# Kernel optimization log

Hardware: AMD Instinct MI355X
Metric: run time of the kernel (lower is better)

The kernel has to match this reference:

```python
import jax, jax.numpy as jnp
import numpy as np

# --- MLA config (DeepSeek-V3 style, scaled) ---
HIDDEN = 4096
N_HEADS = 32
Q_LORA = 1536
KV_LORA = 512
ROPE_D = 64
NOPE_D = 128
V_D = 128
Q_HEAD_D = NOPE_D + ROPE_D  # 192
EPS = 1e-6
SCALING = Q_HEAD_D ** (-0.5)
ROPE_THETA = 10000.0
B, S = 1, 2048


def rms_norm(x, w):
    var = jnp.mean(jnp.square(x.astype(jnp.float32)), axis=-1, keepdims=True)
    return (x * jax.lax.rsqrt(var + EPS)).astype(x.dtype) * w


def rotate_half(x):
    x1, x2 = jnp.split(x, 2, axis=-1)
    return jnp.concatenate([-x2, x1], axis=-1)


def apply_rope(x, cos, sin):
    # x: [B, H, S, ROPE_D]; cos/sin: [B, S, ROPE_D] -> unsqueeze head dim
    c = cos[:, None, :, :]
    s = sin[:, None, :, :]
    return x * c + rotate_half(x) * s


def setup_inputs() -> dict:
    key = jax.random.key(0)
    ks = jax.random.split(key, 8)
    hidden_states = jax.random.normal(ks[0], (B, S, HIDDEN), dtype=jnp.float32)
    # real RoPE tables
    inv_freq = 1.0 / (ROPE_THETA ** (np.arange(0, ROPE_D, 2, dtype=np.float32) / ROPE_D))
    t = np.arange(S, dtype=np.float32)
    freqs = np.outer(t, inv_freq)                      # [S, ROPE_D/2]
    emb = np.concatenate([freqs, freqs], axis=-1)      # [S, ROPE_D]
    cos = jnp.asarray(np.cos(emb))[None].repeat(B, 0)  # [B, S, ROPE_D]
    sin = jnp.asarray(np.sin(emb))[None].repeat(B, 0)
    scale = lambda fan_in: 1.0 / np.sqrt(fan_in)
    w_q_a = jax.random.normal(ks[1], (Q_LORA, HIDDEN), dtype=jnp.float32) * scale(HIDDEN)
    q_a_ln_w = jnp.ones((Q_LORA,), dtype=jnp.float32)
    w_q_b = jax.random.normal(ks[2], (N_HEADS * Q_HEAD_D, Q_LORA), dtype=jnp.float32) * scale(Q_LORA)
    w_kv_a = jax.random.normal(ks[3], (KV_LORA + ROPE_D, HIDDEN), dtype=jnp.float32) * scale(HIDDEN)
    kv_a_ln_w = jnp.ones((KV_LORA,), dtype=jnp.float32)
    w_kv_b = jax.random.normal(ks[4], (N_HEADS * (NOPE_D + V_D), KV_LORA), dtype=jnp.float32) * scale(KV_LORA)
    w_o = jax.random.normal(ks[5], (HIDDEN, N_HEADS * V_D), dtype=jnp.float32) * scale(N_HEADS * V_D)
    return {
        'hidden_states': hidden_states, 'cos': cos, 'sin': sin,
        'w_q_a': w_q_a, 'q_a_ln_w': q_a_ln_w, 'w_q_b': w_q_b,
        'w_kv_a': w_kv_a, 'kv_a_ln_w': kv_a_ln_w, 'w_kv_b': w_kv_b, 'w_o': w_o,
    }


def reference(hidden_states, cos, sin, w_q_a, q_a_ln_w, w_q_b, w_kv_a, kv_a_ln_w, w_kv_b, w_o):
    b, s, _ = hidden_states.shape
    # --- Q path: low-rank down + RMSNorm + up ---
    q_lat = rms_norm(hidden_states @ w_q_a.T, q_a_ln_w)              # [B,S,Q_LORA]
    q = (q_lat @ w_q_b.T).reshape(b, s, N_HEADS, Q_HEAD_D)
    q = q.transpose(0, 2, 1, 3)                                       # [B,H,S,Q_HEAD_D]
    q_nope, q_rot = q[..., :NOPE_D], q[..., NOPE_D:]                  # (note: source names swapped)
    # --- KV path: shared compressed latent + single rotary key ---
    ckv = hidden_states @ w_kv_a.T                                    # [B,S,KV_LORA+ROPE_D]
    k_lat, k_rot = ckv[..., :KV_LORA], ckv[..., KV_LORA:]
    kv = (rms_norm(k_lat, kv_a_ln_w) @ w_kv_b.T).reshape(b, s, N_HEADS, NOPE_D + V_D)
    kv = kv.transpose(0, 2, 1, 3)                                     # [B,H,S,NOPE_D+V_D]
    k_nope, v = kv[..., :NOPE_D], kv[..., NOPE_D:]
    k_rot = k_rot.reshape(b, 1, s, ROPE_D)                            # single rotary key head
    # --- partial RoPE on rotary slices ---
    q_rot = apply_rope(q_rot, cos, sin)
    k_rot = apply_rope(k_rot, cos, sin)
    k_rot = jnp.broadcast_to(k_rot, (b, N_HEADS, s, ROPE_D))
    query = jnp.concatenate([q_rot, q_nope], axis=-1)                 # [B,H,S,192]
    key = jnp.concatenate([k_rot, k_nope], axis=-1)                   # [B,H,S,192]
    # --- eager causal attention ---
    scores = jnp.einsum('bhqd,bhkd->bhqk', query, key) * SCALING
    causal = jnp.tril(jnp.ones((s, s), dtype=bool))
    scores = jnp.where(causal[None, None], scores, jnp.finfo(scores.dtype).min)
    probs = jax.nn.softmax(scores, axis=-1)
    attn = jnp.einsum('bhqk,bhkd->bhqd', probs, v)                    # [B,H,S,V_D]
    attn = attn.transpose(0, 2, 1, 3).reshape(b, s, N_HEADS * V_D)
    return attn @ w_o.T                                               # [B,S,HIDDEN]
```

## Files before the change

### kernel.cpp

```cpp
#include <hip/hip_runtime.h>

typedef unsigned short u16;
typedef u16 u16x4 __attribute__((ext_vector_type(4)));
typedef u16 u16x8 __attribute__((ext_vector_type(8)));
typedef float f32x4 __attribute__((ext_vector_type(4)));
typedef __bf16 bf16x8 __attribute__((ext_vector_type(8)));

#define S_LEN 2048
#define HIDDEN_D 4096
#define NHEADS 32
#define QLORA 1536
#define KVLORA 512
#define ROPED 64
#define NOPED 128
#define VDIM 128
#define QHD 192
#define SCALING_F 0.07216878364870323f

__device__ __forceinline__ u16 f2bf(float x) {
  union { float f; unsigned u; } v; v.f = x;
  unsigned r = v.u + 0x7fffu + ((v.u >> 16) & 1u);
  return (u16)(r >> 16);
}

__device__ __forceinline__ f32x4 mfma_bf16(u16x8 a, u16x8 b, f32x4 c) {
  return __builtin_amdgcn_mfma_f32_16x16x32_bf16(
      __builtin_bit_cast(bf16x8, a), __builtin_bit_cast(bf16x8, b), c, 0, 0, 0);
}

__global__ __launch_bounds__(256) void cvt_kernel(const float* __restrict__ in,
                                                  u16* __restrict__ out, int n4) {
  int i = blockIdx.x * 256 + threadIdx.x;
  if (i >= n4) return;
  f32x4 v = ((const f32x4*)in)[i];
  u16x4 o;
  o[0] = f2bf(v[0]); o[1] = f2bf(v[1]); o[2] = f2bf(v[2]); o[3] = f2bf(v[3]);
  ((u16x4*)out)[i] = o;
}

__global__ __launch_bounds__(256, 2) void gemm_kernel(
    const u16* __restrict__ A, const float* __restrict__ B, float* __restrict__ C,
    int M, int N, int K, int lda, int ldb, int ldc)
{
  __shared__ u16 sA[2][128 * 64];
  __shared__ u16 sB[2][128 * 64];
  const int tid = threadIdx.x;
  const int wid = tid >> 6, lane = tid & 63;
  const int lr = lane & 15, lg = lane >> 4;
  const int nbn = (N + 127) >> 7;
  const int bx = blockIdx.x % nbn, by = blockIdx.x / nbn;
  const int bm = by << 7, bn = bx << 7;
  const int wm = (wid >> 1) << 6, wn = (wid & 1) << 6;

  f32x4 acc[4][4] = {};
  u16x8 areg[4];
  f32x4 br0[4], br1[4];

  auto loadA = [&](int k0) {
#pragma unroll
    for (int i = 0; i < 4; ++i) {
      int chunk = i * 256 + tid;
      int row = chunk >> 3, c8 = chunk & 7;
      int gr = bm + row; if (gr >= M) gr = M - 1;
      areg[i] = *(const u16x8*)(A + (size_t)gr * lda + k0 + (c8 << 3));
    }
  };
  auto loadB = [&](int k0) {
#pragma unroll
    for (int i = 0; i < 4; ++i) {
      int chunk = i * 256 + tid;
      int n = chunk >> 3, c8 = chunk & 7;
      int gn = bn + n; if (gn >= N) gn = N - 1;
      const float* src = B + (size_t)gn * ldb + k0 + (c8 << 3);
      br0[i] = *(const f32x4*)src;
      br1[i] = *(const f32x4*)(src + 4);
    }
  };
  auto writeA = [&](int buf) {
#pragma unroll
    for (int i = 0; i < 4; ++i)
      *(u16x8*)&sA[buf][(i * 256 + tid) * 8] = areg[i];
  };
  auto writeB = [&](int buf) {
#pragma unroll
    for (int i = 0; i < 4; ++i) {
      u16x8 v;
      v[0] = f2bf(br0[i][0]); v[1] = f2bf(br0[i][1]);
      v[2] = f2bf(br0[i][2]); v[3] = f2bf(br0[i][3]);
      v[4] = f2bf(br1[i][0]); v[5] = f2bf(br1[i][1]);
      v[6] = f2bf(br1[i][2]); v[7] = f2bf(br1[i][3]);
      *(u16x8*)&sB[buf][(i * 256 + tid) * 8] = v;
    }
  };
  auto compute = [&](int buf) {
    const u16* pa = sA[buf];
    const u16* pb = sB[buf];
#pragma unroll
    for (int ks = 0; ks < 2; ++ks) {
      const int kof = ks * 32 + lg * 8;
      u16x8 av[4], bv[4];
#pragma unroll
      for (int m = 0; m < 4; ++m) av[m] = *(const u16x8*)&pa[(wm + m * 16 + lr) * 64 + kof];
#pragma unroll
      for (int n = 0; n < 4; ++n) bv[n] = *(const u16x8*)&pb[(wn + n * 16 + lr) * 64 + kof];
#pragma unroll
      for (int m = 0; m < 4; ++m)
#pragma unroll
        for (int n = 0; n < 4; ++n)
          acc[m][n] = mfma_bf16(av[m], bv[n], acc[m][n]);
    }
  };

  const int nk = K >> 6;
  loadA(0); loadB(0);
  writeA(0); writeB(0);
  __syncthreads();
  for (int t = 0; t < nk; ++t) {
    const int cur = t & 1;
    if (t + 1 < nk) { loadA((t + 1) << 6); loadB((t + 1) << 6); }
    compute(cur);
    if (t + 1 < nk) { writeA(cur ^ 1); writeB(cur ^ 1); }
    __syncthreads();
  }
#pragma unroll
  for (int m = 0; m < 4; ++m) {
    const int row0 = bm + wm + m * 16 + (lg << 2);
#pragma unroll
    for (int n = 0; n < 4; ++n) {
      const int col = bn + wn + n * 16 + lr;
      if (col < N) {
#pragma unroll
        for (int r = 0; r < 4; ++r)
          C[(size_t)(row0 + r) * ldc + col] = acc[m][n][r];
      }
    }
  }
}

__global__ __launch_bounds__(256) void rms_kernel(const float* __restrict__ X,
                                                  const float* __restrict__ w,
                                                  u16* __restrict__ out, int D) {
  const int row = blockIdx.x;
  const float* x = X + (size_t)row * D;
  __shared__ float sb[4];
  float ss = 0.f;
  for (int i = threadIdx.x * 4; i < D; i += 1024) {
    f32x4 v = *(const f32x4*)&x[i];
    ss += v[0] * v[0] + v[1] * v[1] + v[2] * v[2] + v[3] * v[3];
  }
#pragma unroll
  for (int off = 32; off >= 1; off >>= 1) ss += __shfl_xor(ss, off, 64);
  if ((threadIdx.x & 63) == 0) sb[threadIdx.x >> 6] = ss;
  __syncthreads();
  const float inv = rsqrtf((sb[0] + sb[1] + sb[2] + sb[3]) / (float)D + 1e-6f);
  u16* o = out + (size_t)row * D;
  for (int i = threadIdx.x * 4; i < D; i += 1024) {
    f32x4 v = *(const f32x4*)&x[i];
    f32x4 wv = *(const f32x4*)&w[i];
    u16x4 u;
    u[0] = f2bf(v[0] * inv * wv[0]); u[1] = f2bf(v[1] * inv * wv[1]);
    u[2] = f2bf(v[2] * inv * wv[2]); u[3] = f2bf(v[3] * inv * wv[3]);
    *(u16x4*)&o[i] = u;
  }
}

__global__ __launch_bounds__(256) void ckv_epi_kernel(const float* __restrict__ ckv,
    const float* __restrict__ w, const float* __restrict__ cosp, const float* __restrict__ sinp,
    u16* __restrict__ klatn, u16* __restrict__ krot) {
  const int s = blockIdx.x;
  const float* x = ckv + (size_t)s * 576;
  __shared__ float sb[4];
  const int i2 = threadIdx.x * 2;
  const float a = x[i2], b = x[i2 + 1];
  float ss = a * a + b * b;
#pragma unroll
  for (int off = 32; off >= 1; off >>= 1) ss += __shfl_xor(ss, off, 64);
  if ((threadIdx.x & 63) == 0) sb[threadIdx.x >> 6] = ss;
  __syncthreads();
  const float inv = rsqrtf((sb[0] + sb[1] + sb[2] + sb[3]) / 512.0f + 1e-6f);
  klatn[(size_t)s * 512 + i2]     = f2bf(a * inv * w[i2]);
  klatn[(size_t)s * 512 + i2 + 1] = f2bf(b * inv * w[i2 + 1]);
  if (threadIdx.x < 64) {
    const int d = threadIdx.x;
    const float xr = x[512 + d];
    const float rr = (d < 32) ? -x[512 + d + 32] : x[512 + d - 32];
    krot[(size_t)s * 64 + d] = f2bf(xr * cosp[s * 64 + d] + rr * sinp[s * 64 + d]);
  }
}

__global__ __launch_bounds__(256) void q_epi_kernel(const float* __restrict__ q_raw,
    const float* __restrict__ cosp, const float* __restrict__ sinp, u16* __restrict__ Qb) {
  const int s = blockIdx.x;
  const float* x = q_raw + (size_t)s * 6144;
  for (int idx = threadIdx.x; idx < 6144; idx += 256) {
    const int h = idx / 192, d = idx - h * 192;
    float v;
    if (d < 64) {
      const float xr = x[h * 192 + 128 + d];
      const float rr = (d < 32) ? -x[h * 192 + 160 + d] : x[h * 192 + 96 + d];
      v = xr * cosp[s * 64 + d] + rr * sinp[s * 64 + d];
    } else {
      v = x[h * 192 + d - 64];
    }
    Qb[((size_t)h * 2048 + s) * QHD + d] = f2bf(v * SCALING_F);
  }
}

__global__ __launch_bounds__(256) void kv_epi_kernel(const float* __restrict__ kv_raw,
    u16* __restrict__ Knope, u16* __restrict__ Vt) {
  const int h = blockIdx.x & 31, st = blockIdx.x >> 5;
  const int s0 = st << 6;
  __shared__ u16 tile[64][VDIM + 2];
  for (int i = 0; i < 32; ++i) {
    const int idx = i * 256 + threadIdx.x;
    const int r = idx >> 7, d = idx & 127;
    const float kn = kv_raw[(size_t)(s0 + r) * 8192 + h * 256 + d];
    Knope[((size_t)h * 2048 + s0 + r) * 128 + d] = f2bf(kn);
    tile[r][d] = f2bf(kv_raw[(size_t)(s0 + r) * 8192 + h * 256 + 128 + d]);
  }
  __syncthreads();
  for (int i = 0; i < 32; ++i) {
    const int idx = i * 256 + threadIdx.x;
    const int d = idx >> 6, r = idx & 63;
    Vt[((size_t)h * 128 + d) * 2048 + s0 + r] = tile[r][d];
  }
}

__global__ __launch_bounds__(256, 2) void flash_kernel(
    const u16* __restrict__ Qb, const u16* __restrict__ Krot,
    const u16* __restrict__ Knope, const u16* __restrict__ Vt,
    u16* __restrict__ attnb)
{
  const int h = blockIdx.x & 31, qt = blockIdx.x >> 5;
  const int q0 = qt << 7;
  __shared__ u16 sK[64][QHD];
  __shared__ u16 sV[VDIM][64];
  __shared__ u16 sP[4][32][64];
  const int tid = threadIdx.x;
  const int wid = tid >> 6, lane = tid & 63;
  const int lr = lane & 15, lg = lane >> 4;

  u16x8 qf[2][6];
#pragma unroll
  for (int m = 0; m < 2; ++m) {
    const int row = q0 + wid * 32 + m * 16 + lr;
#pragma unroll
    for (int kk = 0; kk < 6; ++kk)
      qf[m][kk] = *(const u16x8*)&Qb[((size_t)h * 2048 + row) * QHD + kk * 32 + lg * 8];
  }

  f32x4 acc[2][8] = {};
  float mx[2][4], ls[2][4];
#pragma unroll
  for (int m = 0; m < 2; ++m)
#pragma unroll
    for (int r = 0; r < 4; ++r) { mx[m][r] = -1e30f; ls[m][r] = 0.f; }

  const int nkv = q0 + 128;
  u16x8 kreg[6], vreg[4];

  auto loadKV = [&](int kv0) {
#pragma unroll
    for (int i = 0; i < 6; ++i) {
      const int chunk = i * 256 + tid;
      const int row = chunk / 24, cc = chunk % 24;
      const u16* src = (cc < 8)
          ? &Krot[(size_t)(kv0 + row) * 64 + cc * 8]
          : &Knope[((size_t)h * 2048 + kv0 + row) * 128 + (cc - 8) * 8];
      kreg[i] = *(const u16x8*)src;
    }
#pragma unroll
    for (int i = 0; i < 4; ++i) {
      const int chunk = i * 256 + tid;
      const int d = chunk >> 3, c = chunk & 7;
      vreg[i] = *(const u16x8*)&Vt[((size_t)h * VDIM + d) * 2048 + kv0 + c * 8];
    }
  };

  loadKV(0);
  for (int kv0 = 0; kv0 < nkv; kv0 += 64) {
    __syncthreads();
    u16* kbase = &sK[0][0];
#pragma unroll
    for (int i = 0; i < 6; ++i) *(u16x8*)&kbase[(size_t)(i * 256 + tid) * 8] = kreg[i];
    u16* vbase = &sV[0][0];
#pragma unroll
    for (int i = 0; i < 4; ++i) *(u16x8*)&vbase[(size_t)(i * 256 + tid) * 8] = vreg[i];
    __syncthreads();
    if (kv0 + 64 < nkv) loadKV(kv0 + 64);

    f32x4 sc[2][4] = {};
#pragma unroll
    for (int kk = 0; kk < 6; ++kk) {
      u16x8 bfr[4];
#pragma unroll
      for (int n = 0; n < 4; ++n) bfr[n] = *(const u16x8*)&sK[n * 16 + lr][kk * 32 + lg * 8];
#pragma unroll
      for (int m = 0; m < 2; ++m)
#pragma unroll
        for (int n = 0; n < 4; ++n)
          sc[m][n] = mfma_bf16(qf[m][kk], bfr[n], sc[m][n]);
    }

    if (kv0 + 63 > q0 + wid * 32) {
#pragma unroll
      for (int m = 0; m < 2; ++m)
#pragma unroll
        for (int n = 0; n < 4; ++n) {
          const int kv = kv0 + n * 16 + lr;
#pragma unroll
          for (int r = 0; r < 4; ++r) {
            const int rowq = q0 + wid * 32 + m * 16 + lg * 4 + r;
            if (kv > rowq) sc[m][n][r] = -1e30f;
          }
        }
    }

#pragma unroll
    for (int m = 0; m < 2; ++m) {
      float rs[4];
#pragma unroll
      for (int r = 0; r < 4; ++r) {
        float v = fmaxf(fmaxf(sc[m][0][r], sc[m][1][r]), fmaxf(sc[m][2][r], sc[m][3][r]));
#pragma unroll
        for (int off = 1; off < 16; off <<= 1) v = fmaxf(v, __shfl_xor(v, off, 64));
        const float mnew = fmaxf(mx[m][r], v);
        const float alpha = __expf(mx[m][r] - mnew);
        mx[m][r] = mnew;
        ls[m][r] *= alpha;
#pragma unroll
        for (int df = 0; df < 8; ++df) acc[m][df][r] *= alpha;
        rs[r] = 0.f;
      }
#pragma unroll
      for (int n = 0; n < 4; ++n)
#pragma unroll
        for (int r = 0; r < 4; ++r) {
          const float p = __expf(sc[m][n][r] - mx[m][r]);
          rs[r] += p;
          sP[wid][m * 16 + lg * 4 + r][n * 16 + lr] = f2bf(p);
        }
#pragma unroll
      for (int r = 0; r < 4; ++r) {
        float v = rs[r];
#pragma unroll
        for (int off = 1; off < 16; off <<= 1) v += __shfl_xor(v, off, 64);
        ls[m][r] += v;
      }
    }

#pragma unroll
    for (int ks = 0; ks < 2; ++ks) {
      u16x8 pf0 = *(const u16x8*)&sP[wid][lr][ks * 32 + lg * 8];
      u16x8 pf1 = *(const u16x8*)&sP[wid][16 + lr][ks * 32 + lg * 8];
#pragma unroll
      for (int df = 0; df < 8; ++df) {
        u16x8 vf = *(const u16x8*)&sV[df * 16 + lr][ks * 32 + lg * 8];
        acc[0][df] = mfma_bf16(pf0, vf, acc[0][df]);
        acc[1][df] = mfma_bf16(pf1, vf, acc[1][df]);
      }
    }
  }

#pragma unroll
  for (int m = 0; m < 2; ++m)
#pragma unroll
    for (int df = 0; df < 8; ++df) {
      const int col = h * 128 + df * 16 + lr;
#pragma unroll
      for (int r = 0; r < 4; ++r) {
        const int row = q0 + wid * 32 + m * 16 + lg * 4 + r;
        attnb[(size_t)row * 4096 + col] = f2bf(acc[m][df][r] / ls[m][r]);
      }
    }
}

extern "C" void kernel_launch(void* const* d_in, const int* in_sizes, int n_in,
                              void* d_out, int out_size, void* d_ws, size_t ws_size,
                              hipStream_t stream) {
  (void)in_sizes; (void)n_in; (void)out_size; (void)ws_size;
  const float* hidden  = (const float*)d_in[0];
  const float* cosp    = (const float*)d_in[1];
  const float* sinp    = (const float*)d_in[2];
  const float* w_q_a   = (const float*)d_in[3];
  const float* q_a_ln  = (const float*)d_in[4];
  const float* w_q_b   = (const float*)d_in[5];
  const float* w_kv_a  = (const float*)d_in[6];
  const float* kv_a_ln = (const float*)d_in[7];
  const float* w_kv_b  = (const float*)d_in[8];
  const float* w_o     = (const float*)d_in[9];
  float* out = (float*)d_out;

  char* p = (char*)d_ws;
  auto alloc = [&](size_t bytes) { char* r = p; p += (bytes + 255) & ~(size_t)255; return r; };
  u16* Hb    = (u16*)alloc((size_t)S_LEN * HIDDEN_D * 2);
  u16* qlatn = (u16*)alloc((size_t)S_LEN * QLORA * 2);
  u16* klatn = (u16*)alloc((size_t)S_LEN * KVLORA * 2);
  u16* krot  = (u16*)alloc((size_t)S_LEN * ROPED * 2);
  u16* Qb    = (u16*)alloc((size_t)NHEADS * S_LEN * QHD * 2);
  u16* Knope = (u16*)alloc((size_t)NHEADS * S_LEN * NOPED * 2);
  u16* Vt    = (u16*)alloc((size_t)NHEADS * VDIM * S_LEN * 2);
  u16* attnb = (u16*)alloc((size_t)S_LEN * 4096 * 2);
  float* raw = (float*)alloc((size_t)S_LEN * 8192 * 4);
  float* qlat_raw = raw;
  float* ckv_raw  = raw + (size_t)S_LEN * QLORA;
  float* q_raw    = raw;
  float* kv_raw   = raw;

  cvt_kernel<<<(S_LEN * HIDDEN_D / 4 + 255) / 256, 256, 0, stream>>>(hidden, Hb, S_LEN * HIDDEN_D / 4);
  gemm_kernel<<<16 * 12, 256, 0, stream>>>(Hb, w_q_a, qlat_raw, 2048, 1536, 4096, 4096, 4096, 1536);
  gemm_kernel<<<16 * 5, 256, 0, stream>>>(Hb, w_kv_a, ckv_raw, 2048, 576, 4096, 4096, 4096, 576);
  rms_kernel<<<2048, 256, 0, stream>>>(qlat_raw, q_a_ln, qlatn, 1536);
  ckv_epi_kernel<<<2048, 256, 0, stream>>>(ckv_raw, kv_a_ln, cosp, sinp, klatn, krot);
  gemm_kernel<<<16 * 48, 256, 0, stream>>>(qlatn, w_q_b, q_raw, 2048, 6144, 1536, 1536, 1536, 6144);
  q_epi_kernel<<<2048, 256, 0, stream>>>(q_raw, cosp, sinp, Qb);
  gemm_kernel<<<16 * 64, 256, 0, stream>>>(klatn, w_kv_b, kv_raw, 2048, 8192, 512, 512, 512, 8192);
  kv_epi_kernel<<<1024, 256, 0, stream>>>(kv_raw, Knope, Vt);
  flash_kernel<<<512, 256, 0, stream>>>(Qb, krot, Knope, Vt, attnb);
  gemm_kernel<<<16 * 32, 256, 0, stream>>>(attnb, w_o, out, 2048, 4096, 4096, 4096, 4096, 4096);
}
```

Measured before the change: 680.3 us.

## Pre-convert weights to bf16, use direct-to-LDS GEMM loads, retile flash attention

Adds bf16 conversion kernels for all weight matrices so the GEMM reads bf16 B operands instead of converting fp32 in registers. The GEMM now uses global_load_lds to copy tiles straight into a single LDS buffer, which drops the register double-buffering. Flash attention moves to 64-row query tiles with reversed tile order for causal load balance, XOR-swizzled LDS layouts and setprio around the MFMA sections. The weight conversions run on every call and add memory traffic, and the single-buffered GEMM gives up load/compute overlap. The GEMM bounds clamps were removed, so the kv_a GEMM (N=576) reads weight rows past 576 from the padded 640-row buffer, which is uninitialised.

```diff
diff --git a/kernel.cpp b/kernel.cpp
--- a/kernel.cpp
+++ b/kernel.cpp
@@ -17,6 +17,9 @@
 #define QHD 192
 #define SCALING_F 0.07216878364870323f
 
+#define GLOBAL_U32 const __attribute__((address_space(1))) unsigned int
+#define LDS_U32 __attribute__((address_space(3))) unsigned int
+
 __device__ __forceinline__ u16 f2bf(float x) {
   union { float f; unsigned u; } v; v.f = x;
   unsigned r = v.u + 0x7fffu + ((v.u >> 16) & 1u);
@@ -38,12 +41,12 @@
   ((u16x4*)out)[i] = o;
 }
 
-__global__ __launch_bounds__(256, 2) void gemm_kernel(
-    const u16* __restrict__ A, const float* __restrict__ B, float* __restrict__ C,
+__global__ __launch_bounds__(256, 2) void gemm_bb(
+    const u16* __restrict__ A, const u16* __restrict__ B, float* __restrict__ C,
     int M, int N, int K, int lda, int ldb, int ldc)
 {
-  __shared__ u16 sA[2][128 * 64];
-  __shared__ u16 sB[2][128 * 64];
+  __shared__ u16 sA[128 * 64];
+  __shared__ u16 sB[128 * 64];
   const int tid = threadIdx.x;
   const int wid = tid >> 6, lane = tid & 63;
   const int lr = lane & 15, lg = lane >> 4;
@@ -53,73 +56,39 @@
   const int wm = (wid >> 1) << 6, wn = (wid & 1) << 6;
 
   f32x4 acc[4][4] = {};
-  u16x8 areg[4];
-  f32x4 br0[4], br1[4];
-
-  auto loadA = [&](int k0) {
+
+  const int nk = K >> 6;
+  for (int t = 0; t < nk; ++t) {
+    const int k0 = t << 6;
 #pragma unroll
     for (int i = 0; i < 4; ++i) {
-      int chunk = i * 256 + tid;
-      int row = chunk >> 3, c8 = chunk & 7;
-      int gr = bm + row; if (gr >= M) gr = M - 1;
-      areg[i] = *(const u16x8*)(A + (size_t)gr * lda + k0 + (c8 << 3));
-    }
-  };
-  auto loadB = [&](int k0) {
+      const int chunk = i * 256 + tid;
+      const int row = chunk >> 3, c8 = chunk & 7;
+      const u16* gp = A + (size_t)(bm + row) * lda + k0 + (c8 << 3);
+      __builtin_amdgcn_global_load_lds((GLOBAL_U32*)gp, (LDS_U32*)&sA[chunk * 8], 16, 0, 0);
+    }
 #pragma unroll
     for (int i = 0; i < 4; ++i) {
-      int chunk = i * 256 + tid;
-      int n = chunk >> 3, c8 = chunk & 7;
-      int gn = bn + n; if (gn >= N) gn = N - 1;
-      const float* src = B + (size_t)gn * ldb + k0 + (c8 << 3);
-      br0[i] = *(const f32x4*)src;
-      br1[i] = *(const f32x4*)(src + 4);
-    }
-  };
-  auto writeA = [&](int buf) {
-#pragma unroll
-    for (int i = 0; i < 4; ++i)
-      *(u16x8*)&sA[buf][(i * 256 + tid) * 8] = areg[i];
-  };
-  auto writeB = [&](int buf) {
-#pragma unroll
-    for (int i = 0; i < 4; ++i) {
-      u16x8 v;
-      v[0] = f2bf(br0[i][0]); v[1] = f2bf(br0[i][1]);
-      v[2] = f2bf(br0[i][2]); v[3] = f2bf(br0[i][3]);
-      v[4] = f2bf(br1[i][0]); v[5] = f2bf(br1[i][1]);
-      v[6] = f2bf(br1[i][2]); v[7] = f2bf(br1[i][3]);
-      *(u16x8*)&sB[buf][(i * 256 + tid) * 8] = v;
-    }
-  };
-  auto compute = [&](int buf) {
-    const u16* pa = sA[buf];
-    const u16* pb = sB[buf];
+      const int chunk = i * 256 + tid;
+      const int row = chunk >> 3, c8 = chunk & 7;
+      const u16* gp = B + (size_t)(bn + row) * ldb + k0 + (c8 << 3);
+      __builtin_amdgcn_global_load_lds((GLOBAL_U32*)gp, (LDS_U32*)&sB[chunk * 8], 16, 0, 0);
+    }
+    __syncthreads();
 #pragma unroll
     for (int ks = 0; ks < 2; ++ks) {
       const int kof = ks * 32 + lg * 8;
       u16x8 av[4], bv[4];
 #pragma unroll
-      for (int m = 0; m < 4; ++m) av[m] = *(const u16x8*)&pa[(wm + m * 16 + lr) * 64 + kof];
-#pragma unroll
-      for (int n = 0; n < 4; ++n) bv[n] = *(const u16x8*)&pb[(wn + n * 16 + lr) * 64 + kof];
+      for (int m = 0; m < 4; ++m) av[m] = *(const u16x8*)&sA[(wm + m * 16 + lr) * 64 + kof];
+#pragma unroll
+      for (int n = 0; n < 4; ++n) bv[n] = *(const u16x8*)&sB[(wn + n * 16 + lr) * 64 + kof];
 #pragma unroll
       for (int m = 0; m < 4; ++m)
 #pragma unroll
         for (int n = 0; n < 4; ++n)
           acc[m][n] = mfma_bf16(av[m], bv[n], acc[m][n]);
     }
-  };
-
-  const int nk = K >> 6;
-  loadA(0); loadB(0);
-  writeA(0); writeB(0);
-  __syncthreads();
-  for (int t = 0; t < nk; ++t) {
-    const int cur = t & 1;
-    if (t + 1 < nk) { loadA((t + 1) << 6); loadB((t + 1) << 6); }
-    compute(cur);
-    if (t + 1 < nk) { writeA(cur ^ 1); writeB(cur ^ 1); }
     __syncthreads();
   }
 #pragma unroll
@@ -226,37 +195,36 @@
   }
 }
 
-__global__ __launch_bounds__(256, 2) void flash_kernel(
+__global__ __launch_bounds__(256, 3) void flash_kernel(
     const u16* __restrict__ Qb, const u16* __restrict__ Krot,
     const u16* __restrict__ Knope, const u16* __restrict__ Vt,
     u16* __restrict__ attnb)
 {
-  const int h = blockIdx.x & 31, qt = blockIdx.x >> 5;
-  const int q0 = qt << 7;
-  __shared__ u16 sK[64][QHD];
-  __shared__ u16 sV[VDIM][64];
-  __shared__ u16 sP[4][32][64];
+  const int bid = blockIdx.x;
+  const int h = bid & 31;
+  const int qt = 31 - (bid >> 5);
+  const int q0 = qt << 6;
+  __shared__ u16 sK[64 * QHD];
+  __shared__ u16 sV[VDIM * 64];
+  __shared__ u16 sP[4 * 16 * 64];
   const int tid = threadIdx.x;
   const int wid = tid >> 6, lane = tid & 63;
   const int lr = lane & 15, lg = lane >> 4;
 
-  u16x8 qf[2][6];
-#pragma unroll
-  for (int m = 0; m < 2; ++m) {
-    const int row = q0 + wid * 32 + m * 16 + lr;
-#pragma unroll
-    for (int kk = 0; kk < 6; ++kk)
-      qf[m][kk] = *(const u16x8*)&Qb[((size_t)h * 2048 + row) * QHD + kk * 32 + lg * 8];
-  }
-
-  f32x4 acc[2][8] = {};
-  float mx[2][4], ls[2][4];
-#pragma unroll
-  for (int m = 0; m < 2; ++m)
-#pragma unroll
-    for (int r = 0; r < 4; ++r) { mx[m][r] = -1e30f; ls[m][r] = 0.f; }
-
-  const int nkv = q0 + 128;
+  u16x8 qf[6];
+  {
+    const int row = q0 + wid * 16 + lr;
+    const u16* qp = &Qb[((size_t)h * 2048 + row) * QHD];
+#pragma unroll
+    for (int kk = 0; kk < 6; ++kk) qf[kk] = *(const u16x8*)&qp[kk * 32 + lg * 8];
+  }
+
+  f32x4 acc[8] = {};
+  float mx[4], ls[4];
+#pragma unroll
+  for (int r = 0; r < 4; ++r) { mx[r] = -1e30f; ls[r] = 0.f; }
+
+  const int nkv = q0 + 64;
   u16x8 kreg[6], vreg[4];
 
   auto loadKV = [&](int kv0) {
@@ -278,101 +246,109 @@
   };
 
   loadKV(0);
+  const int pbase = wid * 2048;
   for (int kv0 = 0; kv0 < nkv; kv0 += 64) {
     __syncthreads();
-    u16* kbase = &sK[0][0];
-#pragma unroll
-    for (int i = 0; i < 6; ++i) *(u16x8*)&kbase[(size_t)(i * 256 + tid) * 8] = kreg[i];
-    u16* vbase = &sV[0][0];
-#pragma unroll
-    for (int i = 0; i < 4; ++i) *(u16x8*)&vbase[(size_t)(i * 256 + tid) * 8] = vreg[i];
+#pragma unroll
+    for (int i = 0; i < 6; ++i) {
+      const int chunk = i * 256 + tid;
+      const int row = chunk / 24, cc = chunk % 24;
+      int b = row * 384 + cc * 16; b ^= (row & 7) << 4;
+      *(u16x8*)&sK[b >> 1] = kreg[i];
+    }
+#pragma unroll
+    for (int i = 0; i < 4; ++i) {
+      const int chunk = i * 256 + tid;
+      const int row = chunk >> 3, cc = chunk & 7;
+      int b = row * 128 + cc * 16; b ^= (row & 7) << 4;
+      *(u16x8*)&sV[b >> 1] = vreg[i];
+    }
     __syncthreads();
     if (kv0 + 64 < nkv) loadKV(kv0 + 64);
 
-    f32x4 sc[2][4] = {};
+    f32x4 sc[4] = {};
+    __builtin_amdgcn_s_setprio(1);
 #pragma unroll
     for (int kk = 0; kk < 6; ++kk) {
-      u16x8 bfr[4];
-#pragma unroll
-      for (int n = 0; n < 4; ++n) bfr[n] = *(const u16x8*)&sK[n * 16 + lr][kk * 32 + lg * 8];
-#pragma unroll
-      for (int m = 0; m < 2; ++m)
-#pragma unroll
-        for (int n = 0; n < 4; ++n)
-          sc[m][n] = mfma_bf16(qf[m][kk], bfr[n], sc[m][n]);
-    }
-
-    if (kv0 + 63 > q0 + wid * 32) {
-#pragma unroll
-      for (int m = 0; m < 2; ++m)
-#pragma unroll
-        for (int n = 0; n < 4; ++n) {
-          const int kv = kv0 + n * 16 + lr;
-#pragma unroll
-          for (int r = 0; r < 4; ++r) {
-            const int rowq = q0 + wid * 32 + m * 16 + lg * 4 + r;
-            if (kv > rowq) sc[m][n][r] = -1e30f;
-          }
+#pragma unroll
+      for (int n = 0; n < 4; ++n) {
+        const int row = n * 16 + lr;
+        int b = row * 384 + kk * 64 + lg * 16; b ^= (row & 7) << 4;
+        u16x8 bfr = *(const u16x8*)&sK[b >> 1];
+        sc[n] = mfma_bf16(qf[kk], bfr, sc[n]);
+      }
+    }
+    __builtin_amdgcn_s_setprio(0);
+
+    if (kv0 == q0) {
+#pragma unroll
+      for (int n = 0; n < 4; ++n) {
+        const int kv = kv0 + n * 16 + lr;
+#pragma unroll
+        for (int r = 0; r < 4; ++r) {
+          const int rowq = q0 + wid * 16 + lg * 4 + r;
+          if (kv > rowq) sc[n][r] = -1e30f;
         }
-    }
-
-#pragma unroll
-    for (int m = 0; m < 2; ++m) {
-      float rs[4];
+      }
+    }
+
+    float rs[4];
+#pragma unroll
+    for (int r = 0; r < 4; ++r) {
+      float v = fmaxf(fmaxf(sc[0][r], sc[1][r]), fmaxf(sc[2][r], sc[3][r]));
+#pragma unroll
+      for (int off = 1; off < 16; off <<= 1) v = fmaxf(v, __shfl_xor(v, off, 64));
+      const float mnew = fmaxf(mx[r], v);
+      const float alpha = __expf(mx[r] - mnew);
+      mx[r] = mnew;
+      ls[r] *= alpha;
+#pragma unroll
+      for (int df = 0; df < 8; ++df) acc[df][r] *= alpha;
+      rs[r] = 0.f;
+    }
+#pragma unroll
+    for (int n = 0; n < 4; ++n)
 #pragma unroll
       for (int r = 0; r < 4; ++r) {
-        float v = fmaxf(fmaxf(sc[m][0][r], sc[m][1][r]), fmaxf(sc[m][2][r], sc[m][3][r]));
-#pragma unroll
-        for (int off = 1; off < 16; off <<= 1) v = fmaxf(v, __shfl_xor(v, off, 64));
-        const float mnew = fmaxf(mx[m][r], v);
-        const float alpha = __expf(mx[m][r] - mnew);
-        mx[m][r] = mnew;
-        ls[m][r] *= alpha;
-#pragma unroll
-        for (int df = 0; df < 8; ++df) acc[m][df][r] *= alpha;
-        rs[r] = 0.f;
+        const float p = __expf(sc[n][r] - mx[r]);
+        rs[r] += p;
+        const int prow = lg * 4 + r;
+        int b = prow * 128 + (n * 16 + lr) * 2; b ^= (prow & 7) << 4;
+        sP[(pbase + b) >> 1] = f2bf(p);
       }
 #pragma unroll
-      for (int n = 0; n < 4; ++n)
-#pragma unroll
-        for (int r = 0; r < 4; ++r) {
-          const float p = __expf(sc[m][n][r] - mx[m][r]);
-          rs[r] += p;
-          sP[wid][m * 16 + lg * 4 + r][n * 16 + lr] = f2bf(p);
-        }
-#pragma unroll
-      for (int r = 0; r < 4; ++r) {
-        float v = rs[r];
-#pragma unroll
-        for (int off = 1; off < 16; off <<= 1) v += __shfl_xor(v, off, 64);
-        ls[m][r] += v;
+    for (int r = 0; r < 4; ++r) {
+      float v = rs[r];
+#pragma unroll
+      for (int off = 1; off < 16; off <<= 1) v += __shfl_xor(v, off, 64);
+      ls[r] += v;
+    }
+
+    __builtin_amdgcn_s_setprio(1);
+#pragma unroll
+    for (int ks = 0; ks < 2; ++ks) {
+      int pb = lr * 128 + ks * 64 + lg * 16; pb ^= (lr & 7) << 4;
+      u16x8 pf = *(const u16x8*)&sP[(pbase + pb) >> 1];
+#pragma unroll
+      for (int df = 0; df < 8; ++df) {
+        const int vrow = df * 16 + lr;
+        int vb = vrow * 128 + ks * 64 + lg * 16; vb ^= (vrow & 7) << 4;
+        u16x8 vf = *(const u16x8*)&sV[vb >> 1];
+        acc[df] = mfma_bf16(pf, vf, acc[df]);
       }
     }
-
-#pragma unroll
-    for (int ks = 0; ks < 2; ++ks) {
-      u16x8 pf0 = *(const u16x8*)&sP[wid][lr][ks * 32 + lg * 8];
-      u16x8 pf1 = *(const u16x8*)&sP[wid][16 + lr][ks * 32 + lg * 8];
-#pragma unroll
-      for (int df = 0; df < 8; ++df) {
-        u16x8 vf = *(const u16x8*)&sV[df * 16 + lr][ks * 32 + lg * 8];
-        acc[0][df] = mfma_bf16(pf0, vf, acc[0][df]);
-        acc[1][df] = mfma_bf16(pf1, vf, acc[1][df]);
-      }
-    }
-  }
-
-#pragma unroll
-  for (int m = 0; m < 2; ++m)
-#pragma unroll
-    for (int df = 0; df < 8; ++df) {
-      const int col = h * 128 + df * 16 + lr;
-#pragma unroll
-      for (int r = 0; r < 4; ++r) {
-        const int row = q0 + wid * 32 + m * 16 + lg * 4 + r;
-        attnb[(size_t)row * 4096 + col] = f2bf(acc[m][df][r] / ls[m][r]);
-      }
-    }
+    __builtin_amdgcn_s_setprio(0);
+  }
+
+#pragma unroll
+  for (int df = 0; df < 8; ++df) {
+    const int col = h * 128 + df * 16 + lr;
+#pragma unroll
+    for (int r = 0; r < 4; ++r) {
+      const int row = q0 + wid * 16 + lg * 4 + r;
+      attnb[(size_t)row * 4096 + col] = f2bf(acc[df][r] / ls[r]);
+    }
+  }
 }
 
 extern "C" void kernel_launch(void* const* d_in, const int* in_sizes, int n_in,
@@ -401,6 +377,11 @@
   u16* Knope = (u16*)alloc((size_t)NHEADS * S_LEN * NOPED * 2);
   u16* Vt    = (u16*)alloc((size_t)NHEADS * VDIM * S_LEN * 2);
   u16* attnb = (u16*)alloc((size_t)S_LEN * 4096 * 2);
+  u16* Wqa   = (u16*)alloc((size_t)QLORA * HIDDEN_D * 2);
+  u16* Wqb   = (u16*)alloc((size_t)6144 * QLORA * 2);
+  u16* Wkva  = (u16*)alloc((size_t)640 * HIDDEN_D * 2);
+  u16* Wkvb  = (u16*)alloc((size_t)8192 * KVLORA * 2);
+  u16* Wo    = (u16*)alloc((size_t)HIDDEN_D * 4096 * 2);
   float* raw = (float*)alloc((size_t)S_LEN * 8192 * 4);
   float* qlat_raw = raw;
   float* ckv_raw  = raw + (size_t)S_LEN * QLORA;
@@ -408,14 +389,20 @@
   float* kv_raw   = raw;
 
   cvt_kernel<<<(S_LEN * HIDDEN_D / 4 + 255) / 256, 256, 0, stream>>>(hidden, Hb, S_LEN * HIDDEN_D / 4);
-  gemm_kernel<<<16 * 12, 256, 0, stream>>>(Hb, w_q_a, qlat_raw, 2048, 1536, 4096, 4096, 4096, 1536);
-  gemm_kernel<<<16 * 5, 256, 0, stream>>>(Hb, w_kv_a, ckv_raw, 2048, 576, 4096, 4096, 4096, 576);
+  cvt_kernel<<<(QLORA * HIDDEN_D / 4 + 255) / 256, 256, 0, stream>>>(w_q_a, Wqa, QLORA * HIDDEN_D / 4);
+  cvt_kernel<<<(6144 * QLORA / 4 + 255) / 256, 256, 0, stream>>>(w_q_b, Wqb, 6144 * QLORA / 4);
+  cvt_kernel<<<(576 * HIDDEN_D / 4 + 255) / 256, 256, 0, stream>>>(w_kv_a, Wkva, 576 * HIDDEN_D / 4);
+  cvt_kernel<<<(8192 * KVLORA / 4 + 255) / 256, 256, 0, stream>>>(w_kv_b, Wkvb, 8192 * KVLORA / 4);
+  cvt_kernel<<<(HIDDEN_D * 4096 / 4 + 255) / 256, 256, 0, stream>>>(w_o, Wo, HIDDEN_D * 4096 / 4);
+
+  gemm_bb<<<16 * 12, 256, 0, stream>>>(Hb, Wqa, qlat_raw, 2048, 1536, 4096, 4096, 4096, 1536);
+  gemm_bb<<<16 * 5, 256, 0, stream>>>(Hb, Wkva, ckv_raw, 2048, 576, 4096, 4096, 4096, 576);
   rms_kernel<<<2048, 256, 0, stream>>>(qlat_raw, q_a_ln, qlatn, 1536);
   ckv_epi_kernel<<<2048, 256, 0, stream>>>(ckv_raw, kv_a_ln, cosp, sinp, klatn, krot);
-  gemm_kernel<<<16 * 48, 256, 0, stream>>>(qlatn, w_q_b, q_raw, 2048, 6144, 1536, 1536, 1536, 6144);
+  gemm_bb<<<16 * 48, 256, 0, stream>>>(qlatn, Wqb, q_raw, 2048, 6144, 1536, 1536, 1536, 6144);
   q_epi_kernel<<<2048, 256, 0, stream>>>(q_raw, cosp, sinp, Qb);
-  gemm_kernel<<<16 * 64, 256, 0, stream>>>(klatn, w_kv_b, kv_raw, 2048, 8192, 512, 512, 512, 8192);
+  gemm_bb<<<16 * 64, 256, 0, stream>>>(klatn, Wkvb, kv_raw, 2048, 8192, 512, 512, 512, 8192);
   kv_epi_kernel<<<1024, 256, 0, stream>>>(kv_raw, Knope, Vt);
-  flash_kernel<<<512, 256, 0, stream>>>(Qb, krot, Knope, Vt, attnb);
-  gemm_kernel<<<16 * 32, 256, 0, stream>>>(attnb, w_o, out, 2048, 4096, 4096, 4096, 4096, 4096);
-}
+  flash_kernel<<<1024, 256, 0, stream>>>(Qb, krot, Knope, Vt, attnb);
+  gemm_bb<<<16 * 32, 256, 0, stream>>>(attnb, Wo, out, 2048, 4096, 4096, 4096, 4096, 4096);
+}
```

Measured after the change: 981.4 us. 1.44x slower.
